# Kernel tuning notes

Measured on AMD Instinct MI355X. Metric: run time of the kernel, lower is better.

The kernel has to match this reference:

```python
import jax, jax.numpy as jnp
import numpy as np

E = 1024
H = 16
DH = E // H
EPS = 1e-09


def setup_inputs() -> dict:
    key = jax.random.key(0)
    ks = jax.random.split(key, 12)
    B, S = 2, 2048
    scale = 1.0 / np.sqrt(E)
    inp = {
        "query": jax.random.normal(ks[0], (B, S, E), dtype=jnp.float32),
        "key": jax.random.normal(ks[1], (B, S, E), dtype=jnp.float32),
        "value": jax.random.normal(ks[2], (B, S, E), dtype=jnp.float32),
        "mask": jax.random.randint(ks[3], (B, 1, S, S), 0, 2, dtype=jnp.int32),
        "Wq": jax.random.normal(ks[4], (E, E), dtype=jnp.float32) * scale,
        "bq": jnp.zeros((E,), dtype=jnp.float32),
        "Wk": jax.random.normal(ks[5], (E, E), dtype=jnp.float32) * scale,
        "bk": jnp.zeros((E,), dtype=jnp.float32),
        "Wv": jax.random.normal(ks[6], (E, E), dtype=jnp.float32) * scale,
        "bv": jnp.zeros((E,), dtype=jnp.float32),
        "Wo": jax.random.normal(ks[7], (E, E), dtype=jnp.float32) * scale,
        "bo": jnp.zeros((E,), dtype=jnp.float32),
    }
    return inp


def _split_heads(x):
    # [B,S,E] -> [B,H,S,DH]
    B, S, _ = x.shape
    return x.reshape(B, S, H, DH).transpose(0, 2, 1, 3)


def reference(query, key, value, mask, Wq, bq, Wk, bk, Wv, bv, Wo, bo):
    q = _split_heads(query @ Wq.T + bq)
    k = _split_heads(key @ Wk.T + bk)
    v = _split_heads(value @ Wv.T + bv)
    # scores: [B,H,Sq,Sk]; NOTE: original module applies NO softmax.
    scores = jnp.einsum("bhqd,bhkd->bhqk", q, k) / np.sqrt(DH)
    # masked_fill_(mask == 0, epsilon): replace masked positions with 1e-9
    scores = jnp.where(mask == 0, jnp.float32(EPS), scores)
    # dropout p=0.0 (eval) -> identity
    out = jnp.einsum("bhqk,bhkd->bhqd", scores, v)
    B, _, S, _ = out.shape
    out = out.transpose(0, 2, 1, 3).reshape(B, S, E)
    return out @ Wo.T + bo
```

## Files before the change

kernel.cpp:

```cpp
#include <hip/hip_runtime.h>
#include <hip/hip_bf16.h>
#include <stdint.h>
#include <stddef.h>

#define SB 2
#define SS 2048
#define SE 1024
#define SH 16
#define SD 64

typedef __attribute__((ext_vector_type(8))) short bf16x8;
typedef __attribute__((ext_vector_type(4))) float f32x4;

__device__ __forceinline__ short f2bf(float f) {
    union { float f; uint32_t u; } v; v.f = f;
    uint32_t u = v.u;
    uint32_t r = (u + 0x7fffu + ((u >> 16) & 1u)) >> 16;
    return (short)(uint16_t)r;
}

__device__ __forceinline__ uint32_t pkmask(float a, float b, uint32_t bits) {
    union { float f; uint32_t u; } ua, ub;
    ua.f = a; ub.f = b;
    uint32_t ra = (bits & 1u) ? (ua.u + 0x7fffu + ((ua.u >> 16) & 1u)) : 0u;
    uint32_t rb = (bits & 2u) ? (ub.u + 0x7fffu + ((ub.u >> 16) & 1u)) : 0u;
    return (rb & 0xffff0000u) | (ra >> 16);
}

__device__ __forceinline__ void gld16(const short* g, short* l) {
    __builtin_amdgcn_global_load_lds(
        (const __attribute__((address_space(1))) unsigned int*)g,
        (__attribute__((address_space(3))) unsigned int*)l, 16, 0, 0);
}

struct CvtArgs {
    const float* src[7];
    short* dst[7];
    int nblk[7];
};

__global__ __launch_bounds__(256) void cvt_bf16(CvtArgs a) {
    const int j = blockIdx.y;
    if (blockIdx.x >= a.nblk[j]) return;
    const size_t i = ((size_t)blockIdx.x * 256 + threadIdx.x) * 8;
    const float* s = a.src[j] + i;
    f32x4 f0 = *(const f32x4*)s;
    f32x4 f1 = *(const f32x4*)(s + 4);
    bf16x8 o;
    o[0] = f2bf(f0[0]); o[1] = f2bf(f0[1]); o[2] = f2bf(f0[2]); o[3] = f2bf(f0[3]);
    o[4] = f2bf(f1[0]); o[5] = f2bf(f1[1]); o[6] = f2bf(f1[2]); o[7] = f2bf(f1[3]);
    *(bf16x8*)(a.dst[j] + i) = o;
}

__global__ __launch_bounds__(256) void pack_mask(const int* __restrict__ m,
                                                 unsigned long long* __restrict__ mp) {
    const int lane = threadIdx.x & 63;
    int wv = (blockIdx.x * 256 + threadIdx.x) >> 6;
    const int NW = SB * SS * (SS / 64);
    const int stride = (gridDim.x * 256) >> 6;
    for (int wd = wv; wd < NW; wd += stride) {
        int v = m[(size_t)wd * 64 + lane];
        unsigned long long bb = __ballot(v != 0);
        if (lane == 0) {
            int b = wd >> 16;
            int q = (wd >> 5) & 2047;
            int kw = wd & 31;
            mp[((size_t)b << 16) + kw * 2048 + q] = bb;
        }
    }
}

struct GemmJob {
    const short* A; const short* W; const float* bias; void* C;
    int mode;
    float scale;
};

template <bool OUTF32>
__global__ __launch_bounds__(256, 3) void gemm128(GemmJob j0, GemmJob j1, GemmJob j2) {
    GemmJob j = (blockIdx.z == 0) ? j0 : (blockIdx.z == 1) ? j1 : j2;
    __shared__ short As[128 * 64];
    __shared__ short Bs[128 * 64];

    const int m0 = blockIdx.y * 128;
    const int n0 = blockIdx.x * 128;
    const int tid = threadIdx.x;
    const int lane = tid & 63;
    const int w = tid >> 6;
    const int wm = (w >> 1) * 64;
    const int wn = (w & 1) * 64;
    const int quad = lane >> 4;
    const int l16 = lane & 15;

    f32x4 acc[4][4] = {};

    for (int k0 = 0; k0 < 1024; k0 += 64) {
#pragma unroll
        for (int i = 0; i < 4; ++i) {
            int ch = lane + 64 * (w * 4 + i);
            int row = ch >> 3;
            int col = (ch & 7) * 8;
            gld16(j.A + (size_t)(m0 + row) * 1024 + k0 + col, &As[(w * 4 + i) * 512]);
            gld16(j.W + (size_t)(n0 + row) * 1024 + k0 + col, &Bs[(w * 4 + i) * 512]);
        }
        __syncthreads();
#pragma unroll
        for (int ks = 0; ks < 2; ++ks) {
            bf16x8 af[4], bfr[4];
#pragma unroll
            for (int mi = 0; mi < 4; ++mi)
                af[mi] = *(const bf16x8*)&As[(wm + mi * 16 + l16) * 64 + ks * 32 + quad * 8];
#pragma unroll
            for (int ni = 0; ni < 4; ++ni)
                bfr[ni] = *(const bf16x8*)&Bs[(wn + ni * 16 + l16) * 64 + ks * 32 + quad * 8];
#pragma unroll
            for (int mi = 0; mi < 4; ++mi)
#pragma unroll
                for (int ni = 0; ni < 4; ++ni)
                    acc[mi][ni] = __builtin_amdgcn_mfma_f32_16x16x32_bf16(
                        af[mi], bfr[ni], acc[mi][ni], 0, 0, 0);
        }
        __syncthreads();
    }

#pragma unroll
    for (int mi = 0; mi < 4; ++mi) {
#pragma unroll
        for (int ni = 0; ni < 4; ++ni) {
            int n = n0 + wn + ni * 16 + l16;
            float bv = j.bias[n];
#pragma unroll
            for (int r = 0; r < 4; ++r) {
                int m = m0 + wm + mi * 16 + quad * 4 + r;
                float v = (acc[mi][ni][r] + bv) * j.scale;
                if (OUTF32) {
                    ((float*)j.C)[(size_t)m * 1024 + n] = v;
                } else {
                    short o = f2bf(v);
                    short* C = (short*)j.C;
                    if (j.mode == 0) {
                        C[(size_t)m * 1024 + n] = o;
                    } else {
                        int b = m >> 11, s = m & 2047;
                        int hh = n >> 6, d = n & 63;
                        if (j.mode == 1)
                            C[(((size_t)(b * SH + hh) * SS) + s) * SD + d] = o;
                        else
                            C[(((size_t)(b * SH + hh) * SD) + d) * SS + s] = o;
                    }
                }
            }
        }
    }
}

__global__ __launch_bounds__(256, 4) void attn2(
    const short* __restrict__ Q,
    const short* __restrict__ Kk,
    const short* __restrict__ Vt,
    const unsigned long long* __restrict__ MpT,
    short* __restrict__ O) {
    __shared__ __align__(16) short Ks[2][64 * 72];
    __shared__ __align__(16) short Vs[2][64 * 72];

    const int qt = blockIdx.x;
    const int bh = blockIdx.y;
    const int b = bh >> 4;
    const int h = bh & 15;
    const int q0 = qt * 64;

    const short* qbase = Q + (size_t)bh * SS * SD;
    const short* kbase = Kk + (size_t)bh * SS * SD;
    const short* vbase = Vt + (size_t)bh * SD * SS;
    const unsigned long long* mTb = MpT + ((size_t)b << 16);

    const int tid = threadIdx.x;
    const int lane = tid & 63;
    const int w = tid >> 6;
    const int quad = lane >> 4;
    const int l16 = lane & 15;
    const int qw = q0 + w * 16;

    const bf16x8 qf0 = *(const bf16x8*)(qbase + (size_t)(qw + l16) * SD + quad * 8);
    const bf16x8 qf1 = *(const bf16x8*)(qbase + (size_t)(qw + l16) * SD + 32 + quad * 8);

    f32x4 oacc[4] = {};

    bf16x8 kpf[2], vpf[2];
    int prow[2], pcol[2];
#pragma unroll
    for (int r = 0; r < 2; ++r) {
        int ch = tid + r * 256;
        prow[r] = ch >> 3;
        pcol[r] = (ch & 7) * 8;
    }
    auto loadKV = [&](int k0) {
#pragma unroll
        for (int r = 0; r < 2; ++r) {
            kpf[r] = *(const bf16x8*)(kbase + (size_t)(k0 + prow[r]) * SD + pcol[r]);
            vpf[r] = *(const bf16x8*)(vbase + (size_t)prow[r] * SS + k0 + pcol[r]);
        }
    };
    auto storeKV = [&](int buf) {
#pragma unroll
        for (int r = 0; r < 2; ++r) {
            *(bf16x8*)&Ks[buf][prow[r] * 72 + pcol[r]] = kpf[r];
            *(bf16x8*)&Vs[buf][prow[r] * 72 + pcol[r]] = vpf[r];
        }
    };

    loadKV(0);
    int cur = 0;

    for (int k0 = 0; k0 < SS; k0 += 64) {
        storeKV(cur);
        if (k0 + 64 < SS) loadKV(k0 + 64);
        unsigned long long w64 = mTb[(k0 >> 6) * 2048 + qw + l16];
        __syncthreads();

        const short* KsB = &Ks[cur][0];
        const short* VsB = &Vs[cur][0];
#pragma unroll
        for (int p = 0; p < 2; ++p) {
            const int s0 = p * 2, s1 = p * 2 + 1;
            bf16x8 a00 = *(const bf16x8*)&KsB[(s0 * 16 + l16) * 72 + quad * 8];
            bf16x8 a01 = *(const bf16x8*)&KsB[(s0 * 16 + l16) * 72 + 32 + quad * 8];
            bf16x8 a10 = *(const bf16x8*)&KsB[(s1 * 16 + l16) * 72 + quad * 8];
            bf16x8 a11 = *(const bf16x8*)&KsB[(s1 * 16 + l16) * 72 + 32 + quad * 8];
            f32x4 sA = {}, sB = {};
            sA = __builtin_amdgcn_mfma_f32_16x16x32_bf16(a00, qf0, sA, 0, 0, 0);
            sA = __builtin_amdgcn_mfma_f32_16x16x32_bf16(a01, qf1, sA, 0, 0, 0);
            sB = __builtin_amdgcn_mfma_f32_16x16x32_bf16(a10, qf0, sB, 0, 0, 0);
            sB = __builtin_amdgcn_mfma_f32_16x16x32_bf16(a11, qf1, sB, 0, 0, 0);

            uint32_t sh0 = (uint32_t)(w64 >> (s0 * 16 + quad * 4));
            uint32_t sh1 = (uint32_t)(w64 >> (s1 * 16 + quad * 4));
            union { uint32_t d[4]; bf16x8 v; } scf;
            scf.d[0] = pkmask(sA[0], sA[1], sh0);
            scf.d[1] = pkmask(sA[2], sA[3], sh0 >> 2);
            scf.d[2] = pkmask(sB[0], sB[1], sh1);
            scf.d[3] = pkmask(sB[2], sB[3], sh1 >> 2);

#pragma unroll
            for (int di = 0; di < 4; ++di) {
                union { uint32_t d[4]; bf16x8 v; } vb;
                const uint32_t* vlo =
                    (const uint32_t*)&VsB[(di * 16 + l16) * 72 + s0 * 16 + quad * 4];
                const uint32_t* vhi =
                    (const uint32_t*)&VsB[(di * 16 + l16) * 72 + s1 * 16 + quad * 4];
                vb.d[0] = vlo[0]; vb.d[1] = vlo[1];
                vb.d[2] = vhi[0]; vb.d[3] = vhi[1];
                oacc[di] = __builtin_amdgcn_mfma_f32_16x16x32_bf16(
                    scf.v, vb.v, oacc[di], 0, 0, 0);
            }
        }
        cur ^= 1;
    }

#pragma unroll
    for (int di = 0; di < 4; ++di) {
        int d = di * 16 + l16;
#pragma unroll
        for (int r = 0; r < 4; ++r) {
            int qg = qw + quad * 4 + r;
            O[((size_t)b * SS + qg) * SE + h * SD + d] = f2bf(oacc[di][r]);
        }
    }
}

extern "C" void kernel_launch(void* const* d_in, const int* in_sizes, int n_in,
                              void* d_out, int out_size, void* d_ws,
                              size_t ws_size, hipStream_t stream) {
    const float* query = (const float*)d_in[0];
    const float* key   = (const float*)d_in[1];
    const float* value = (const float*)d_in[2];
    const int*   mask  = (const int*)d_in[3];
    float* out = (float*)d_out;

    const size_t NEL = (size_t)SB * SS * SE;
    unsigned long long* Mp = (unsigned long long*)d_out;
    short* mb   = (short*)d_in[3];
    short* qbf  = mb;
    short* kbf  = mb + NEL;
    short* vbf  = mb + 2 * NEL;
    short* Wqb  = mb + 3 * NEL;
    short* Wkb  = Wqb + SE * SE;
    short* Wvb  = Wkb + SE * SE;
    short* Wob  = Wvb + SE * SE;
    short* Qb   = (short*)d_in[0];
    short* Om   = (short*)d_in[0] + NEL;
    short* Kb   = (short*)d_in[1];
    short* Vtb  = (short*)d_in[2];

    dim3 tblk(256);

    pack_mask<<<dim3(1024), tblk, 0, stream>>>(mask, Mp);

    CvtArgs ca;
    ca.src[0] = query; ca.dst[0] = qbf; ca.nblk[0] = 2048;
    ca.src[1] = key;   ca.dst[1] = kbf; ca.nblk[1] = 2048;
    ca.src[2] = value; ca.dst[2] = vbf; ca.nblk[2] = 2048;
    ca.src[3] = (const float*)d_in[4];  ca.dst[3] = Wqb; ca.nblk[3] = 512;
    ca.src[4] = (const float*)d_in[6];  ca.dst[4] = Wkb; ca.nblk[4] = 512;
    ca.src[5] = (const float*)d_in[8];  ca.dst[5] = Wvb; ca.nblk[5] = 512;
    ca.src[6] = (const float*)d_in[10]; ca.dst[6] = Wob; ca.nblk[6] = 512;
    cvt_bf16<<<dim3(2048, 7), tblk, 0, stream>>>(ca);

    GemmJob jq{qbf, Wqb, (const float*)d_in[5], Qb,  1, 0.125f};
    GemmJob jv{vbf, Wvb, (const float*)d_in[9], Vtb, 2, 1.0f};
    GemmJob jk{kbf, Wkb, (const float*)d_in[7], Kb,  1, 1.0f};
    gemm128<false><<<dim3(8, 32, 3), tblk, 0, stream>>>(jq, jv, jk);

    attn2<<<dim3(SS / 64, SB * SH), tblk, 0, stream>>>(Qb, Kb, Vtb, Mp, Om);

    GemmJob jo{Om, Wob, (const float*)d_in[11], out, 0, 1.0f};
    gemm128<true><<<dim3(8, 32, 1), tblk, 0, stream>>>(jo, jo, jo);
}
```

Measured before the change: 287.0 us.

## Process two 16-row query tiles per wave in attention kernel

```diff
diff --git a/kernel.cpp b/kernel.cpp
--- a/kernel.cpp
+++ b/kernel.cpp
@@ -154,7 +154,7 @@
     }
 }
 
-__global__ __launch_bounds__(256, 4) void attn2(
+__global__ __launch_bounds__(256, 2) void attn2(
     const short* __restrict__ Q,
     const short* __restrict__ Kk,
     const short* __restrict__ Vt,
@@ -167,7 +167,6 @@
     const int bh = blockIdx.y;
     const int b = bh >> 4;
     const int h = bh & 15;
-    const int q0 = qt * 64;
 
     const short* qbase = Q + (size_t)bh * SS * SD;
     const short* kbase = Kk + (size_t)bh * SS * SD;
@@ -179,12 +178,16 @@
     const int w = tid >> 6;
     const int quad = lane >> 4;
     const int l16 = lane & 15;
-    const int qw = q0 + w * 16;
-
-    const bf16x8 qf0 = *(const bf16x8*)(qbase + (size_t)(qw + l16) * SD + quad * 8);
-    const bf16x8 qf1 = *(const bf16x8*)(qbase + (size_t)(qw + l16) * SD + 32 + quad * 8);
-
-    f32x4 oacc[4] = {};
+    const int qw = qt * 128 + w * 32;
+
+    bf16x8 qf[2][2];
+#pragma unroll
+    for (int u = 0; u < 2; ++u) {
+        qf[u][0] = *(const bf16x8*)(qbase + (size_t)(qw + u * 16 + l16) * SD + quad * 8);
+        qf[u][1] = *(const bf16x8*)(qbase + (size_t)(qw + u * 16 + l16) * SD + 32 + quad * 8);
+    }
+
+    f32x4 oacc[2][4] = {};
 
     bf16x8 kpf[2], vpf[2];
     int prow[2], pcol[2];
@@ -215,7 +218,8 @@
     for (int k0 = 0; k0 < SS; k0 += 64) {
         storeKV(cur);
         if (k0 + 64 < SS) loadKV(k0 + 64);
-        unsigned long long w64 = mTb[(k0 >> 6) * 2048 + qw + l16];
+        unsigned long long wq0 = mTb[(k0 >> 6) * 2048 + qw + l16];
+        unsigned long long wq1 = mTb[(k0 >> 6) * 2048 + qw + 16 + l16];
         __syncthreads();
 
         const short* KsB = &Ks[cur][0];
@@ -227,19 +231,24 @@
             bf16x8 a01 = *(const bf16x8*)&KsB[(s0 * 16 + l16) * 72 + 32 + quad * 8];
             bf16x8 a10 = *(const bf16x8*)&KsB[(s1 * 16 + l16) * 72 + quad * 8];
             bf16x8 a11 = *(const bf16x8*)&KsB[(s1 * 16 + l16) * 72 + 32 + quad * 8];
-            f32x4 sA = {}, sB = {};
-            sA = __builtin_amdgcn_mfma_f32_16x16x32_bf16(a00, qf0, sA, 0, 0, 0);
-            sA = __builtin_amdgcn_mfma_f32_16x16x32_bf16(a01, qf1, sA, 0, 0, 0);
-            sB = __builtin_amdgcn_mfma_f32_16x16x32_bf16(a10, qf0, sB, 0, 0, 0);
-            sB = __builtin_amdgcn_mfma_f32_16x16x32_bf16(a11, qf1, sB, 0, 0, 0);
-
-            uint32_t sh0 = (uint32_t)(w64 >> (s0 * 16 + quad * 4));
-            uint32_t sh1 = (uint32_t)(w64 >> (s1 * 16 + quad * 4));
-            union { uint32_t d[4]; bf16x8 v; } scf;
-            scf.d[0] = pkmask(sA[0], sA[1], sh0);
-            scf.d[1] = pkmask(sA[2], sA[3], sh0 >> 2);
-            scf.d[2] = pkmask(sB[0], sB[1], sh1);
-            scf.d[3] = pkmask(sB[2], sB[3], sh1 >> 2);
+
+            union SCU { uint32_t d[4]; bf16x8 v; } scf[2];
+#pragma unroll
+            for (int u = 0; u < 2; ++u) {
+                f32x4 sA = {}, sB = {};
+                sA = __builtin_amdgcn_mfma_f32_16x16x32_bf16(a00, qf[u][0], sA, 0, 0, 0);
+                sA = __builtin_amdgcn_mfma_f32_16x16x32_bf16(a01, qf[u][1], sA, 0, 0, 0);
+                sB = __builtin_amdgcn_mfma_f32_16x16x32_bf16(a10, qf[u][0], sB, 0, 0, 0);
+                sB = __builtin_amdgcn_mfma_f32_16x16x32_bf16(a11, qf[u][1], sB, 0, 0, 0);
+
+                unsigned long long w64 = u ? wq1 : wq0;
+                uint32_t sh0 = (uint32_t)(w64 >> (s0 * 16 + quad * 4));
+                uint32_t sh1 = (uint32_t)(w64 >> (s1 * 16 + quad * 4));
+                scf[u].d[0] = pkmask(sA[0], sA[1], sh0);
+                scf[u].d[1] = pkmask(sA[2], sA[3], sh0 >> 2);
+                scf[u].d[2] = pkmask(sB[0], sB[1], sh1);
+                scf[u].d[3] = pkmask(sB[2], sB[3], sh1 >> 2);
+            }
 
 #pragma unroll
             for (int di = 0; di < 4; ++di) {
@@ -250,20 +259,25 @@
                     (const uint32_t*)&VsB[(di * 16 + l16) * 72 + s1 * 16 + quad * 4];
                 vb.d[0] = vlo[0]; vb.d[1] = vlo[1];
                 vb.d[2] = vhi[0]; vb.d[3] = vhi[1];
-                oacc[di] = __builtin_amdgcn_mfma_f32_16x16x32_bf16(
-                    scf.v, vb.v, oacc[di], 0, 0, 0);
+                oacc[0][di] = __builtin_amdgcn_mfma_f32_16x16x32_bf16(
+                    scf[0].v, vb.v, oacc[0][di], 0, 0, 0);
+                oacc[1][di] = __builtin_amdgcn_mfma_f32_16x16x32_bf16(
+                    scf[1].v, vb.v, oacc[1][di], 0, 0, 0);
             }
         }
         cur ^= 1;
     }
 
 #pragma unroll
-    for (int di = 0; di < 4; ++di) {
-        int d = di * 16 + l16;
-#pragma unroll
-        for (int r = 0; r < 4; ++r) {
-            int qg = qw + quad * 4 + r;
-            O[((size_t)b * SS + qg) * SE + h * SD + d] = f2bf(oacc[di][r]);
+    for (int u = 0; u < 2; ++u) {
+#pragma unroll
+        for (int di = 0; di < 4; ++di) {
+            int d = di * 16 + l16;
+#pragma unroll
+            for (int r = 0; r < 4; ++r) {
+                int qg2 = qw + u * 16 + quad * 4 + r;
+                O[((size_t)b * SS + qg2) * SE + h * SD + d] = f2bf(oacc[u][di][r]);
+            }
         }
     }
 }
@@ -311,8 +325,10 @@
     GemmJob jk{kbf, Wkb, (const float*)d_in[7], Kb,  1, 1.0f};
     gemm128<false><<<dim3(8, 32, 3), tblk, 0, stream>>>(jq, jv, jk);
 
-    attn2<<<dim3(SS / 64, SB * SH), tblk, 0, stream>>>(Qb, Kb, Vtb, Mp, Om);
-
-    GemmJob jo{Om, Wob, (const float*)d_in[11], out, 0, 1.0f};
-    gemm128<true><<<dim3(8, 32, 1), tblk, 0, stream>>>(jo, jo, jo);
-}
+    attn2<<<dim3(SS / 128, SB * SH), tblk, 0, stream>>>(Qb, Kb, Vtb, Mp, Om);
+
+    gemm128<true><<<dim3(8, 32, 1), tblk, 0, stream>>>(
+        GemmJob{Om, Wob, (const float*)d_in[11], out, 0, 1.0f},
+        GemmJob{Om, Wob, (const float*)d_in[11], out, 0, 1.0f},
+        GemmJob{Om, Wob, (const float*)d_in[11], out, 0, 1.0f});
+}
```

After: 279.0 us. -2.8%, faster.
